# Optimization experiments

Measured on AMD Instinct MI355X. Metric: run time of the kernel, lower is better.

The kernel has to match this reference:

```python
import jax, jax.numpy as jnp
import numpy as np

H = 16  # hidden_size
D = 32  # input_size == output_size
B = 2048
T = 512


def _leaky(x):
    return jnp.where(x >= 0, x, 0.01 * x)  # nn.LeakyReLU default slope


def _lstm_cell(x, h, c, Wih, Whh, bih, bhh):
    # torch.nn.LSTMCell gate order: i, f, g, o
    g = x @ Wih.T + h @ Whh.T + bih + bhh  # [B, 4H]
    i, f, gg, o = jnp.split(g, 4, axis=-1)
    i = jax.nn.sigmoid(i)
    f = jax.nn.sigmoid(f)
    gg = jnp.tanh(gg)
    o = jax.nn.sigmoid(o)
    c = f * c + i * gg
    h = o * jnp.tanh(c)
    return h, c


def setup_inputs() -> dict:
    key = jax.random.key(0)
    ks = jax.random.split(key, 20)
    s = 1.0 / np.sqrt(H)
    u = lambda k, shape: jax.random.uniform(k, shape, jnp.float32, -s, s)
    return {
        "seq": jax.random.normal(ks[0], (B, T, D), jnp.float32),
        "pre_w1": u(ks[1], (H, D)), "pre_b1": u(ks[2], (H,)),
        "pre_w2": u(ks[3], (H, H)), "pre_b2": u(ks[4], (H,)),
        "pre_w3": u(ks[5], (H, H)), "pre_b3": u(ks[6], (H,)),
        "enc_Wih": u(ks[7], (4 * H, H)), "enc_Whh": u(ks[8], (4 * H, H)),
        "enc_bih": u(ks[9], (4 * H,)), "enc_bhh": u(ks[10], (4 * H,)),
        "h2l_w1": u(ks[11], (H, H)), "h2l_b1": u(ks[12], (H,)),
        "h2l_w2": u(ks[13], (H, H)), "h2l_b2": u(ks[14], (H,)),
        "post_w": u(ks[15], (D, H)), "post_b": u(ks[16], (D,)),
    }


def reference(seq, pre_w1, pre_b1, pre_w2, pre_b2, pre_w3, pre_b3,
              enc_Wih, enc_Whh, enc_bih, enc_bhh,
              h2l_w1, h2l_b1, h2l_w2, h2l_b2, post_w, post_b):
    Bx = seq.shape[0]
    # pre MLP: Linear -> LeakyReLU -> Linear -> LeakyReLU -> Linear
    x = _leaky(seq @ pre_w1.T + pre_b1)
    x = _leaky(x @ pre_w2.T + pre_b2)
    x = x @ pre_w3.T + pre_b3  # [B, T, H]

    start0 = x[:, -1, :]
    h0 = jnp.zeros((Bx, H), seq.dtype)
    c0 = jnp.zeros((Bx, H), seq.dtype)

    # encoder loop over time (serial)
    def enc_step(carry, xt):
        h, c = carry
        h, c = _lstm_cell(xt, h, c, enc_Wih, enc_Whh, enc_bih, enc_bhh)
        return (h, c), None

    (h, c), _ = jax.lax.scan(enc_step, (h0, c0), jnp.swapaxes(x, 0, 1))

    # decoder loop (note: source reuses self.encoder cell here)
    def dec_step(carry, _):
        h, c, start = carry
        h, c = _lstm_cell(start, h, c, enc_Wih, enc_Whh, enc_bih, enc_bhh)
        start = _leaky(h @ h2l_w1.T + h2l_b1) @ h2l_w2.T + h2l_b2
        out = h @ post_w.T + post_b  # [B, D]
        return (h, c, start), out

    _, outs = jax.lax.scan(dec_step, (h, c, start0), None, length=seq.shape[1])
    # outputs[:, -1 - i] = out_i  ->  reverse time, then [B, T, D]
    outputs = jnp.swapaxes(outs[::-1], 0, 1)
    return (outputs, outputs)
```

## Files before the change

### kernel.cpp

```cpp
#include <hip/hip_runtime.h>

#define T_LEN 512
#define OSTRIDE ((size_t)2048 * 512 * 32)

typedef float v2f __attribute__((ext_vector_type(2)));
#define PKFMA(a, b, c) __builtin_elementwise_fma((a), (b), (c))

__device__ __forceinline__ float rlf(float v, int l) {
  return __int_as_float(__builtin_amdgcn_readlane(__float_as_int(v), l));
}
#define QB(v, pat) __int_as_float(__builtin_amdgcn_mov_dpp(__float_as_int(v), (pat), 0xF, 0xF, false))

__global__ __launch_bounds__(64) void setup_kernel(
    const float* __restrict__ Wih, const float* __restrict__ bih,
    const float* __restrict__ bhh, const float* __restrict__ w3,
    const float* __restrict__ b3, float* __restrict__ Wz,
    float* __restrict__ Bz) {
  const int g = threadIdx.x;
  const float sK = ((g >> 4) == 2) ? 2.0f : -1.0f;
  float acc[16];
#pragma unroll
  for (int k = 0; k < 16; ++k) acc[k] = 0.f;
  float bz = bih[g] + bhh[g];
#pragma unroll
  for (int j = 0; j < 16; ++j) {
    const float wij = Wih[g * 16 + j];
#pragma unroll
    for (int k = 0; k < 16; ++k)
      acc[k] = __builtin_fmaf(wij, w3[j * 16 + k], acc[k]);
    bz = __builtin_fmaf(wij, b3[j], bz);
  }
#pragma unroll
  for (int k = 0; k < 16; ++k) Wz[g * 16 + k] = sK * acc[k];
  Bz[g] = sK * bz;
}

__global__ __launch_bounds__(256) void prenet_y2_kernel(
    const float* __restrict__ seq,
    const float* __restrict__ w1, const float* __restrict__ b1,
    const float* __restrict__ w2, const float* __restrict__ b2,
    const float* __restrict__ w3, const float* __restrict__ b3,
    float* __restrict__ y2g, float* __restrict__ xstart) {
  const int tid = threadIdx.x;
  const size_t r = (size_t)blockIdx.x * 256 + tid;

  const float* sp = seq + r * 32;
  float in[32];
#pragma unroll
  for (int q = 0; q < 8; ++q) {
    float4 v = ((const float4*)sp)[q];
    in[q * 4 + 0] = v.x;
    in[q * 4 + 1] = v.y;
    in[q * 4 + 2] = v.z;
    in[q * 4 + 3] = v.w;
  }

  float y1[16];
#pragma unroll
  for (int j = 0; j < 16; ++j) {
    float a0 = b1[j], a1 = 0.f, a2 = 0.f, a3 = 0.f;
#pragma unroll
    for (int k = 0; k < 32; k += 4) {
      a0 = __builtin_fmaf(w1[j * 32 + k + 0], in[k + 0], a0);
      a1 = __builtin_fmaf(w1[j * 32 + k + 1], in[k + 1], a1);
      a2 = __builtin_fmaf(w1[j * 32 + k + 2], in[k + 2], a2);
      a3 = __builtin_fmaf(w1[j * 32 + k + 3], in[k + 3], a3);
    }
    float s = (a0 + a1) + (a2 + a3);
    y1[j] = s >= 0.f ? s : 0.01f * s;
  }

  float y2[16];
#pragma unroll
  for (int j = 0; j < 16; ++j) {
    float a0 = b2[j], a1 = 0.f, a2 = 0.f, a3 = 0.f;
#pragma unroll
    for (int k = 0; k < 16; k += 4) {
      a0 = __builtin_fmaf(w2[j * 16 + k + 0], y1[k + 0], a0);
      a1 = __builtin_fmaf(w2[j * 16 + k + 1], y1[k + 1], a1);
      a2 = __builtin_fmaf(w2[j * 16 + k + 2], y1[k + 2], a2);
      a3 = __builtin_fmaf(w2[j * 16 + k + 3], y1[k + 3], a3);
    }
    float s = (a0 + a1) + (a2 + a3);
    y2[j] = s >= 0.f ? s : 0.01f * s;
  }

  float* op = y2g + r * 16;
#pragma unroll
  for (int q = 0; q < 4; ++q)
    ((float4*)op)[q] = make_float4(y2[q * 4 + 0], y2[q * 4 + 1],
                                   y2[q * 4 + 2], y2[q * 4 + 3]);

  if ((r & (T_LEN - 1)) == (T_LEN - 1)) {
    float y3[16];
#pragma unroll
    for (int j = 0; j < 16; ++j) {
      float a0 = b3[j], a1 = 0.f, a2 = 0.f, a3 = 0.f;
#pragma unroll
      for (int k = 0; k < 16; k += 4) {
        a0 = __builtin_fmaf(w3[j * 16 + k + 0], y2[k + 0], a0);
        a1 = __builtin_fmaf(w3[j * 16 + k + 1], y2[k + 1], a1);
        a2 = __builtin_fmaf(w3[j * 16 + k + 2], y2[k + 2], a2);
        a3 = __builtin_fmaf(w3[j * 16 + k + 3], y2[k + 3], a3);
      }
      y3[j] = (a0 + a1) + (a2 + a3);
    }
    float* xs = xstart + (r >> 9) * 16;
#pragma unroll
    for (int q = 0; q < 4; ++q)
      ((float4*)xs)[q] = make_float4(y3[q * 4 + 0], y3[q * 4 + 1],
                                     y3[q * 4 + 2], y3[q * 4 + 3]);
  }
}

#define ACTBODY()                                                           \
  do {                                                                      \
    float ee = __expf(g);                                                   \
    float rr = __builtin_amdgcn_rcpf(1.0f + ee);                            \
    float act = __builtin_fmaf(sa, rr, sb);                                 \
    float ii = QB(act, 0x00);                                               \
    float ff = QB(act, 0x55);                                               \
    float gg = QB(act, 0xAA);                                               \
    float oo = QB(act, 0xFF);                                               \
    c = __builtin_fmaf(ff, c, ii * gg);                                     \
    float th = __builtin_fmaf(                                              \
        -2.0f, __builtin_amdgcn_rcpf(1.0f + __expf(c + c)), 1.0f);          \
    h = oo * th;                                                            \
    _Pragma("unroll") for (int m = 0; m < 8; ++m) {                         \
      hk2[m].x = rlf(h, 8 * m);                                             \
      hk2[m].y = rlf(h, 8 * m + 4);                                         \
    }                                                                       \
  } while (0)

#define CELLZ(ZV)                                                           \
  do {                                                                      \
    v2f A, Bv;                                                              \
    A.x = (ZV); A.y = 0.f; Bv.x = 0.f; Bv.y = 0.f;                          \
    _Pragma("unroll") for (int m = 0; m < 8; m += 2) {                      \
      A = PKFMA(whh2[m], hk2[m], A);                                        \
      Bv = PKFMA(whh2[m + 1], hk2[m + 1], Bv);                              \
    }                                                                       \
    float g = (A.x + A.y) + (Bv.x + Bv.y);                                  \
    ACTBODY();                                                              \
  } while (0)

#define CELL(WX2, XA2, BB)                                                  \
  do {                                                                      \
    v2f A, Bv;                                                              \
    A.x = (BB); A.y = 0.f; Bv.x = 0.f; Bv.y = 0.f;                          \
    _Pragma("unroll") for (int m = 0; m < 8; m += 2) {                      \
      A = PKFMA(WX2[m], XA2[m], A);                                         \
      Bv = PKFMA(WX2[m + 1], XA2[m + 1], Bv);                               \
    }                                                                       \
    _Pragma("unroll") for (int m = 0; m < 8; m += 2) {                      \
      A = PKFMA(whh2[m], hk2[m], A);                                        \
      Bv = PKFMA(whh2[m + 1], hk2[m + 1], Bv);                              \
    }                                                                       \
    float g = (A.x + A.y) + (Bv.x + Bv.y);                                  \
    ACTBODY();                                                              \
  } while (0)

#define ZGEMV(YQ, OUTV)                                                     \
  do {                                                                      \
    v2f A, Bv;                                                              \
    A.x = bz; A.y = 0.f; Bv.x = 0.f; Bv.y = 0.f;                            \
    _Pragma("unroll") for (int q = 0; q < 4; ++q) {                         \
      float4 v = (YQ)[q];                                                   \
      v2f ylo, yhi;                                                         \
      ylo.x = v.x; ylo.y = v.y; yhi.x = v.z; yhi.y = v.w;                   \
      A = PKFMA(wz2[2 * q + 0], ylo, A);                                    \
      Bv = PKFMA(wz2[2 * q + 1], yhi, Bv);                                  \
    }                                                                       \
    OUTV = (A.x + A.y) + (Bv.x + Bv.y);                                     \
  } while (0)

__global__ __launch_bounds__(256, 2) void lstm_rec_z_kernel(
    const float* __restrict__ Whh, const float* __restrict__ Wih,
    const float* __restrict__ bih, const float* __restrict__ bhh,
    const float* __restrict__ hw1, const float* __restrict__ hb1,
    const float* __restrict__ hw2, const float* __restrict__ hb2,
    const float* __restrict__ pw, const float* __restrict__ pb,
    const float* __restrict__ Wz, const float* __restrict__ Bz,
    const float* __restrict__ y2g, const float* __restrict__ xstart,
    float* __restrict__ out) {
  const int lane = threadIdx.x & 63;
  const int bu =
      __builtin_amdgcn_readfirstlane(blockIdx.x * 4 + (threadIdx.x >> 6));
  const int hr = lane >> 2;
  const int gi = (lane & 3) * 16 + hr;
  const bool isT = (lane & 3) == 2;

  const float sK = isT ? 2.0f : -1.0f;
  const float sa = isT ? -2.0f : 1.0f;
  const float sb = isT ? 1.0f : 0.0f;

  v2f whh2[8];
#pragma unroll
  for (int m = 0; m < 8; ++m) {
    whh2[m].x = Whh[gi * 16 + 2 * m + 0] * sK;
    whh2[m].y = Whh[gi * 16 + 2 * m + 1] * sK;
  }

  v2f wz2[8];
  {
    const float4* wzv = (const float4*)(Wz + gi * 16);
#pragma unroll
    for (int q = 0; q < 4; ++q) {
      float4 v = wzv[q];
      wz2[2 * q + 0].x = v.x;
      wz2[2 * q + 0].y = v.y;
      wz2[2 * q + 1].x = v.z;
      wz2[2 * q + 1].y = v.w;
    }
  }
  const float bz = Bz[gi];

  float h = 0.f, c = 0.f;
  v2f hk2[8];
#pragma unroll
  for (int m = 0; m < 8; ++m) { hk2[m].x = 0.f; hk2[m].y = 0.f; }

  const float4* yb = (const float4*)(y2g + (size_t)bu * (T_LEN * 16));
  float4 yq[4][4];
#pragma unroll
  for (int u = 0; u < 4; ++u) {
#pragma unroll
    for (int q = 0; q < 4; ++q) yq[u][q] = yb[u * 4 + q];
  }
  __builtin_amdgcn_sched_barrier(0);

  float zcur;
  ZGEMV(yq[0], zcur);

  for (int t0 = 0; t0 < T_LEN; t0 += 4) {
#pragma unroll
    for (int u = 0; u < 4; ++u) {
      float znext;
      ZGEMV(yq[(u + 1) & 3], znext);
      CELLZ(zcur);
      int tn = t0 + u + 4;
      tn = tn < T_LEN ? tn : (T_LEN - 1);
#pragma unroll
      for (int q = 0; q < 4; ++q) yq[u][q] = yb[(size_t)tn * 4 + q];
      __builtin_amdgcn_sched_barrier(0);
      zcur = znext;
    }
  }

  v2f wih2[8];
#pragma unroll
  for (int m = 0; m < 8; ++m) {
    wih2[m].x = Wih[gi * 16 + 2 * m + 0] * sK;
    wih2[m].y = Wih[gi * 16 + 2 * m + 1] * sK;
  }
  const float bias = (bih[gi] + bhh[gi]) * sK;

  const int mrow = (lane < 32) ? lane : (lane & 15);
  const float* msrc = (lane < 32) ? (pw + mrow * 16) : (hw1 + mrow * 16);
  const float mbias = (lane < 32) ? pb[mrow] : hb1[mrow];
  const float sl = (lane < 32) ? 1.0f : 0.01f;
  v2f mr2[8];
#pragma unroll
  for (int m = 0; m < 8; ++m) {
    mr2[m].x = msrc[2 * m + 0];
    mr2[m].y = msrc[2 * m + 1];
  }

  float Mr[16];
#pragma unroll
  for (int k = 0; k < 16; ++k) Mr[k] = 0.f;
#pragma unroll
  for (int j = 0; j < 16; ++j) {
    const float wj = (j & 1) ? wih2[j >> 1].y : wih2[j >> 1].x;
#pragma unroll
    for (int k = 0; k < 16; ++k)
      Mr[k] = __builtin_fmaf(wj, hw2[j * 16 + k], Mr[k]);
  }
  float mbias2 = bias;
#pragma unroll
  for (int j = 0; j < 16; ++j) {
    const float wj = (j & 1) ? wih2[j >> 1].y : wih2[j >> 1].x;
    mbias2 = __builtin_fmaf(wj, hb2[j], mbias2);
  }
  v2f Mr2[8];
#pragma unroll
  for (int m = 0; m < 8; ++m) {
    Mr2[m].x = Mr[2 * m + 0];
    Mr2[m].y = Mr[2 * m + 1];
  }

  v2f xk2[8];
  {
    const float* src = xstart + (size_t)bu * 16;
#pragma unroll
    for (int m = 0; m < 8; ++m) {
      xk2[m].x = src[2 * m + 0];
      xk2[m].y = src[2 * m + 1];
    }
  }

  const size_t obase = (size_t)bu * (T_LEN * 32) + (lane & 31);

  CELL(wih2, xk2, bias);

  for (int t = 0; t < T_LEN; ++t) {
    v2f P, Q;
    P.x = mbias; P.y = 0.f; Q.x = 0.f; Q.y = 0.f;
#pragma unroll
    for (int m = 0; m < 8; m += 2) {
      P = PKFMA(mr2[m], hk2[m], P);
      Q = PKFMA(mr2[m + 1], hk2[m + 1], Q);
    }
    float y0 = (P.x + P.y) + (Q.x + Q.y);
    float yv = fmaxf(y0, y0 * sl);

    if (lane < 32) {
      const size_t off = obase + (size_t)(T_LEN - 1 - t) * 32;
      out[off] = yv;
      out[off + OSTRIDE] = yv;
    }

    if (t + 1 < T_LEN) {
      v2f uk2[8];
#pragma unroll
      for (int m = 0; m < 8; ++m) {
        uk2[m].x = rlf(yv, 32 + 2 * m + 0);
        uk2[m].y = rlf(yv, 32 + 2 * m + 1);
      }
      CELL(Mr2, uk2, mbias2);
    }
  }
}

__device__ __forceinline__ void prenet_row(
    const float* __restrict__ sp,
    const float* __restrict__ w1, const float* __restrict__ b1,
    const float* __restrict__ w2, const float* __restrict__ b2,
    const float* __restrict__ w3, const float* __restrict__ b3,
    float y3[16]) {
  float in[32];
#pragma unroll
  for (int q = 0; q < 8; ++q) {
    float4 v = ((const float4*)sp)[q];
    in[q * 4 + 0] = v.x;
    in[q * 4 + 1] = v.y;
    in[q * 4 + 2] = v.z;
    in[q * 4 + 3] = v.w;
  }
  float y1[16];
#pragma unroll
  for (int j = 0; j < 16; ++j) {
    float a0 = b1[j], a1 = 0.f, a2 = 0.f, a3 = 0.f;
#pragma unroll
    for (int k = 0; k < 32; k += 4) {
      a0 = __builtin_fmaf(w1[j * 32 + k + 0], in[k + 0], a0);
      a1 = __builtin_fmaf(w1[j * 32 + k + 1], in[k + 1], a1);
      a2 = __builtin_fmaf(w1[j * 32 + k + 2], in[k + 2], a2);
      a3 = __builtin_fmaf(w1[j * 32 + k + 3], in[k + 3], a3);
    }
    float s = (a0 + a1) + (a2 + a3);
    y1[j] = s >= 0.f ? s : 0.01f * s;
  }
  float y2[16];
#pragma unroll
  for (int j = 0; j < 16; ++j) {
    float a0 = b2[j], a1 = 0.f, a2 = 0.f, a3 = 0.f;
#pragma unroll
    for (int k = 0; k < 16; k += 4) {
      a0 = __builtin_fmaf(w2[j * 16 + k + 0], y1[k + 0], a0);
      a1 = __builtin_fmaf(w2[j * 16 + k + 1], y1[k + 1], a1);
      a2 = __builtin_fmaf(w2[j * 16 + k + 2], y1[k + 2], a2);
      a3 = __builtin_fmaf(w2[j * 16 + k + 3], y1[k + 3], a3);
    }
    float s = (a0 + a1) + (a2 + a3);
    y2[j] = s >= 0.f ? s : 0.01f * s;
  }
#pragma unroll
  for (int j = 0; j < 16; ++j) {
    float a0 = b3[j], a1 = 0.f, a2 = 0.f, a3 = 0.f;
#pragma unroll
    for (int k = 0; k < 16; k += 4) {
      a0 = __builtin_fmaf(w3[j * 16 + k + 0], y2[k + 0], a0);
      a1 = __builtin_fmaf(w3[j * 16 + k + 1], y2[k + 1], a1);
      a2 = __builtin_fmaf(w3[j * 16 + k + 2], y2[k + 2], a2);
      a3 = __builtin_fmaf(w3[j * 16 + k + 3], y2[k + 3], a3);
    }
    y3[j] = (a0 + a1) + (a2 + a3);
  }
}

__global__ __launch_bounds__(256) void prenet_kernel(
    const float* __restrict__ seq,
    const float* __restrict__ w1, const float* __restrict__ b1,
    const float* __restrict__ w2, const float* __restrict__ b2,
    const float* __restrict__ w3, const float* __restrict__ b3,
    float* __restrict__ xws) {
  const size_t r = (size_t)blockIdx.x * 256 + threadIdx.x;
  float y3[16];
  prenet_row(seq + r * 32, w1, b1, w2, b2, w3, b3, y3);
  float* op = xws + r * 16;
#pragma unroll
  for (int q = 0; q < 4; ++q)
    ((float4*)op)[q] =
        make_float4(y3[q * 4 + 0], y3[q * 4 + 1], y3[q * 4 + 2], y3[q * 4 + 3]);
}

__global__ __launch_bounds__(256, 2) void lstm_rec_kernel(
    const float* __restrict__ Wih, const float* __restrict__ Whh,
    const float* __restrict__ bih, const float* __restrict__ bhh,
    const float* __restrict__ hw1, const float* __restrict__ hb1,
    const float* __restrict__ hw2, const float* __restrict__ hb2,
    const float* __restrict__ pw, const float* __restrict__ pb,
    const float* __restrict__ xws, float* __restrict__ out) {
  const int lane = threadIdx.x & 63;
  const int bu =
      __builtin_amdgcn_readfirstlane(blockIdx.x * 4 + (threadIdx.x >> 6));
  const int hr = lane >> 2;
  const int gi = (lane & 3) * 16 + hr;
  const bool isT = (lane & 3) == 2;

  const float sK = isT ? 2.0f : -1.0f;
  const float sa = isT ? -2.0f : 1.0f;
  const float sb = isT ? 1.0f : 0.0f;

  v2f wih2[8], whh2[8];
#pragma unroll
  for (int m = 0; m < 8; ++m) {
    wih2[m].x = Wih[gi * 16 + 2 * m + 0] * sK;
    wih2[m].y = Wih[gi * 16 + 2 * m + 1] * sK;
    whh2[m].x = Whh[gi * 16 + 2 * m + 0] * sK;
    whh2[m].y = Whh[gi * 16 + 2 * m + 1] * sK;
  }
  const float bias = (bih[gi] + bhh[gi]) * sK;

  float h = 0.f, c = 0.f;
  v2f hk2[8];
#pragma unroll
  for (int m = 0; m < 8; ++m) { hk2[m].x = 0.f; hk2[m].y = 0.f; }

  const float* xb = xws + (size_t)bu * (T_LEN * 16);

  v2f xA2[8], xB2[8];
#pragma unroll
  for (int m = 0; m < 8; ++m) {
    xA2[m].x = xb[2 * m + 0];
    xA2[m].y = xb[2 * m + 1];
  }
  for (int t = 0; t < T_LEN; t += 2) {
    const float* n1 = xb + (size_t)(t + 1) * 16;
#pragma unroll
    for (int m = 0; m < 8; ++m) {
      xB2[m].x = n1[2 * m + 0];
      xB2[m].y = n1[2 * m + 1];
    }
    CELL(wih2, xA2, bias);
    const int t2 = (t + 2 < T_LEN) ? (t + 2) : (T_LEN - 1);
    const float* n2 = xb + (size_t)t2 * 16;
#pragma unroll
    for (int m = 0; m < 8; ++m) {
      xA2[m].x = n2[2 * m + 0];
      xA2[m].y = n2[2 * m + 1];
    }
    CELL(wih2, xB2, bias);
  }

  const int mrow = (lane < 32) ? lane : (lane & 15);
  const float* msrc = (lane < 32) ? (pw + mrow * 16) : (hw1 + mrow * 16);
  const float mbias = (lane < 32) ? pb[mrow] : hb1[mrow];
  const float sl = (lane < 32) ? 1.0f : 0.01f;
  v2f mr2[8];
#pragma unroll
  for (int m = 0; m < 8; ++m) {
    mr2[m].x = msrc[2 * m + 0];
    mr2[m].y = msrc[2 * m + 1];
  }

  float Mr[16];
#pragma unroll
  for (int k = 0; k < 16; ++k) Mr[k] = 0.f;
#pragma unroll
  for (int j = 0; j < 16; ++j) {
    const float wj = (j & 1) ? wih2[j >> 1].y : wih2[j >> 1].x;
#pragma unroll
    for (int k = 0; k < 16; ++k)
      Mr[k] = __builtin_fmaf(wj, hw2[j * 16 + k], Mr[k]);
  }
  float mbias2 = bias;
#pragma unroll
  for (int j = 0; j < 16; ++j) {
    const float wj = (j & 1) ? wih2[j >> 1].y : wih2[j >> 1].x;
    mbias2 = __builtin_fmaf(wj, hb2[j], mbias2);
  }
  v2f Mr2[8];
#pragma unroll
  for (int m = 0; m < 8; ++m) {
    Mr2[m].x = Mr[2 * m + 0];
    Mr2[m].y = Mr[2 * m + 1];
  }

  v2f xk2[8];
  {
    const float* src = xb + (size_t)(T_LEN - 1) * 16;
#pragma unroll
    for (int m = 0; m < 8; ++m) {
      xk2[m].x = src[2 * m + 0];
      xk2[m].y = src[2 * m + 1];
    }
  }

  const size_t obase = (size_t)bu * (T_LEN * 32) + (lane & 31);

  CELL(wih2, xk2, bias);

  for (int t = 0; t < T_LEN; ++t) {
    v2f P, Q;
    P.x = mbias; P.y = 0.f; Q.x = 0.f; Q.y = 0.f;
#pragma unroll
    for (int m = 0; m < 8; m += 2) {
      P = PKFMA(mr2[m], hk2[m], P);
      Q = PKFMA(mr2[m + 1], hk2[m + 1], Q);
    }
    float y0 = (P.x + P.y) + (Q.x + Q.y);
    float yv = fmaxf(y0, y0 * sl);

    if (lane < 32) {
      const size_t off = obase + (size_t)(T_LEN - 1 - t) * 32;
      out[off] = yv;
      out[off + OSTRIDE] = yv;
    }

    if (t + 1 < T_LEN) {
      v2f uk2[8];
#pragma unroll
      for (int m = 0; m < 8; ++m) {
        uk2[m].x = rlf(yv, 32 + 2 * m + 0);
        uk2[m].y = rlf(yv, 32 + 2 * m + 1);
      }
      CELL(Mr2, uk2, mbias2);
    }
  }
}

extern "C" void kernel_launch(void* const* d_in, const int* in_sizes, int n_in,
                              void* d_out, int out_size, void* d_ws, size_t ws_size,
                              hipStream_t stream) {
  const float* seq = (const float*)d_in[0];
  const float* pre_w1 = (const float*)d_in[1];
  const float* pre_b1 = (const float*)d_in[2];
  const float* pre_w2 = (const float*)d_in[3];
  const float* pre_b2 = (const float*)d_in[4];
  const float* pre_w3 = (const float*)d_in[5];
  const float* pre_b3 = (const float*)d_in[6];
  const float* enc_Wih = (const float*)d_in[7];
  const float* enc_Whh = (const float*)d_in[8];
  const float* enc_bih = (const float*)d_in[9];
  const float* enc_bhh = (const float*)d_in[10];
  const float* h2l_w1 = (const float*)d_in[11];
  const float* h2l_b1 = (const float*)d_in[12];
  const float* h2l_w2 = (const float*)d_in[13];
  const float* h2l_b2 = (const float*)d_in[14];
  const float* post_w = (const float*)d_in[15];
  const float* post_b = (const float*)d_in[16];

  const size_t y2bytes = (size_t)2048 * 512 * 16 * 4;
  const size_t xsbytes = (size_t)2048 * 16 * 4;
  const size_t wzbytes = 64 * 16 * 4;
  const size_t need = y2bytes + xsbytes + wzbytes + 64 * 4;

  if (ws_size >= need) {
    float* y2g = (float*)d_ws;
    float* xstart = (float*)((char*)d_ws + y2bytes);
    float* Wz = (float*)((char*)d_ws + y2bytes + xsbytes);
    float* Bz = (float*)((char*)d_ws + y2bytes + xsbytes + wzbytes);

    setup_kernel<<<dim3(1), dim3(64), 0, stream>>>(
        enc_Wih, enc_bih, enc_bhh, pre_w3, pre_b3, Wz, Bz);

    prenet_y2_kernel<<<dim3(4096), dim3(256), 0, stream>>>(
        seq, pre_w1, pre_b1, pre_w2, pre_b2, pre_w3, pre_b3, y2g, xstart);

    lstm_rec_z_kernel<<<dim3(512), dim3(256), 0, stream>>>(
        enc_Whh, enc_Wih, enc_bih, enc_bhh, h2l_w1, h2l_b1, h2l_w2, h2l_b2,
        post_w, post_b, Wz, Bz, y2g, xstart, (float*)d_out);
  } else {
    float* xws = (float*)d_ws;

    prenet_kernel<<<dim3(4096), dim3(256), 0, stream>>>(
        seq, pre_w1, pre_b1, pre_w2, pre_b2, pre_w3, pre_b3, xws);

    lstm_rec_kernel<<<dim3(512), dim3(256), 0, stream>>>(
        enc_Wih, enc_Whh, enc_bih, enc_bhh, h2l_w1, h2l_b1, h2l_w2, h2l_b2,
        post_w, post_b, xws, (float*)d_out);
  }
}
```

Before: 712.9 us.

## Fuse prenet MLP into recurrent LSTM kernel with per-wave LDS chunks

Replaces the separate setup and prenet kernels, and the global y2 workspace, with a single kernel. Each wave computes the first two prenet layers for its own batch row in chunks of 128 timesteps, stages them in LDS, and then runs the encoder recurrence from LDS. The folded Wih·W3 weights and the decoder start vector are now computed inside the kernel. This removes the large global round trip for y2 and two kernel launches. In exchange, the prenet work now runs inside each latency-bound recurrence wave instead of a wide parallel kernel, and the kernel uses more LDS and registers.

```diff
diff --git a/kernel.cpp b/kernel.cpp
--- a/kernel.cpp
+++ b/kernel.cpp
@@ -11,107 +11,6 @@
 }
 #define QB(v, pat) __int_as_float(__builtin_amdgcn_mov_dpp(__float_as_int(v), (pat), 0xF, 0xF, false))
 
-__global__ __launch_bounds__(64) void setup_kernel(
-    const float* __restrict__ Wih, const float* __restrict__ bih,
-    const float* __restrict__ bhh, const float* __restrict__ w3,
-    const float* __restrict__ b3, float* __restrict__ Wz,
-    float* __restrict__ Bz) {
-  const int g = threadIdx.x;
-  const float sK = ((g >> 4) == 2) ? 2.0f : -1.0f;
-  float acc[16];
-#pragma unroll
-  for (int k = 0; k < 16; ++k) acc[k] = 0.f;
-  float bz = bih[g] + bhh[g];
-#pragma unroll
-  for (int j = 0; j < 16; ++j) {
-    const float wij = Wih[g * 16 + j];
-#pragma unroll
-    for (int k = 0; k < 16; ++k)
-      acc[k] = __builtin_fmaf(wij, w3[j * 16 + k], acc[k]);
-    bz = __builtin_fmaf(wij, b3[j], bz);
-  }
-#pragma unroll
-  for (int k = 0; k < 16; ++k) Wz[g * 16 + k] = sK * acc[k];
-  Bz[g] = sK * bz;
-}
-
-__global__ __launch_bounds__(256) void prenet_y2_kernel(
-    const float* __restrict__ seq,
-    const float* __restrict__ w1, const float* __restrict__ b1,
-    const float* __restrict__ w2, const float* __restrict__ b2,
-    const float* __restrict__ w3, const float* __restrict__ b3,
-    float* __restrict__ y2g, float* __restrict__ xstart) {
-  const int tid = threadIdx.x;
-  const size_t r = (size_t)blockIdx.x * 256 + tid;
-
-  const float* sp = seq + r * 32;
-  float in[32];
-#pragma unroll
-  for (int q = 0; q < 8; ++q) {
-    float4 v = ((const float4*)sp)[q];
-    in[q * 4 + 0] = v.x;
-    in[q * 4 + 1] = v.y;
-    in[q * 4 + 2] = v.z;
-    in[q * 4 + 3] = v.w;
-  }
-
-  float y1[16];
-#pragma unroll
-  for (int j = 0; j < 16; ++j) {
-    float a0 = b1[j], a1 = 0.f, a2 = 0.f, a3 = 0.f;
-#pragma unroll
-    for (int k = 0; k < 32; k += 4) {
-      a0 = __builtin_fmaf(w1[j * 32 + k + 0], in[k + 0], a0);
-      a1 = __builtin_fmaf(w1[j * 32 + k + 1], in[k + 1], a1);
-      a2 = __builtin_fmaf(w1[j * 32 + k + 2], in[k + 2], a2);
-      a3 = __builtin_fmaf(w1[j * 32 + k + 3], in[k + 3], a3);
-    }
-    float s = (a0 + a1) + (a2 + a3);
-    y1[j] = s >= 0.f ? s : 0.01f * s;
-  }
-
-  float y2[16];
-#pragma unroll
-  for (int j = 0; j < 16; ++j) {
-    float a0 = b2[j], a1 = 0.f, a2 = 0.f, a3 = 0.f;
-#pragma unroll
-    for (int k = 0; k < 16; k += 4) {
-      a0 = __builtin_fmaf(w2[j * 16 + k + 0], y1[k + 0], a0);
-      a1 = __builtin_fmaf(w2[j * 16 + k + 1], y1[k + 1], a1);
-      a2 = __builtin_fmaf(w2[j * 16 + k + 2], y1[k + 2], a2);
-      a3 = __builtin_fmaf(w2[j * 16 + k + 3], y1[k + 3], a3);
-    }
-    float s = (a0 + a1) + (a2 + a3);
-    y2[j] = s >= 0.f ? s : 0.01f * s;
-  }
-
-  float* op = y2g + r * 16;
-#pragma unroll
-  for (int q = 0; q < 4; ++q)
-    ((float4*)op)[q] = make_float4(y2[q * 4 + 0], y2[q * 4 + 1],
-                                   y2[q * 4 + 2], y2[q * 4 + 3]);
-
-  if ((r & (T_LEN - 1)) == (T_LEN - 1)) {
-    float y3[16];
-#pragma unroll
-    for (int j = 0; j < 16; ++j) {
-      float a0 = b3[j], a1 = 0.f, a2 = 0.f, a3 = 0.f;
-#pragma unroll
-      for (int k = 0; k < 16; k += 4) {
-        a0 = __builtin_fmaf(w3[j * 16 + k + 0], y2[k + 0], a0);
-        a1 = __builtin_fmaf(w3[j * 16 + k + 1], y2[k + 1], a1);
-        a2 = __builtin_fmaf(w3[j * 16 + k + 2], y2[k + 2], a2);
-        a3 = __builtin_fmaf(w3[j * 16 + k + 3], y2[k + 3], a3);
-      }
-      y3[j] = (a0 + a1) + (a2 + a3);
-    }
-    float* xs = xstart + (r >> 9) * 16;
-#pragma unroll
-    for (int q = 0; q < 4; ++q)
-      ((float4*)xs)[q] = make_float4(y3[q * 4 + 0], y3[q * 4 + 1],
-                                     y3[q * 4 + 2], y3[q * 4 + 3]);
-  }
-}
 
 #define ACTBODY()                                                           \
   do {                                                                      \
@@ -174,18 +73,66 @@
     OUTV = (A.x + A.y) + (Bv.x + Bv.y);                                     \
   } while (0)
 
-__global__ __launch_bounds__(256, 2) void lstm_rec_z_kernel(
-    const float* __restrict__ Whh, const float* __restrict__ Wih,
+#define PHASEA_ROW(SR, ROWOFF)                                              \
+  do {                                                                      \
+    float in[32];                                                           \
+    _Pragma("unroll") for (int q = 0; q < 8; ++q) {                         \
+      in[q * 4 + 0] = SR[q].x;                                              \
+      in[q * 4 + 1] = SR[q].y;                                              \
+      in[q * 4 + 2] = SR[q].z;                                              \
+      in[q * 4 + 3] = SR[q].w;                                              \
+    }                                                                       \
+    float y1[16];                                                           \
+    _Pragma("unroll") for (int j = 0; j < 16; ++j) {                        \
+      float a0 = b1[j], a1 = 0.f, a2 = 0.f, a3 = 0.f;                       \
+      _Pragma("unroll") for (int k = 0; k < 32; k += 4) {                   \
+        a0 = __builtin_fmaf(w1[j * 32 + k + 0], in[k + 0], a0);             \
+        a1 = __builtin_fmaf(w1[j * 32 + k + 1], in[k + 1], a1);             \
+        a2 = __builtin_fmaf(w1[j * 32 + k + 2], in[k + 2], a2);             \
+        a3 = __builtin_fmaf(w1[j * 32 + k + 3], in[k + 3], a3);             \
+      }                                                                     \
+      float s = (a0 + a1) + (a2 + a3);                                      \
+      y1[j] = s >= 0.f ? s : 0.01f * s;                                     \
+    }                                                                       \
+    float y2[16];                                                           \
+    _Pragma("unroll") for (int j = 0; j < 16; ++j) {                        \
+      float a0 = b2[j], a1 = 0.f, a2 = 0.f, a3 = 0.f;                       \
+      _Pragma("unroll") for (int k = 0; k < 16; k += 4) {                   \
+        a0 = __builtin_fmaf(w2[j * 16 + k + 0], y1[k + 0], a0);             \
+        a1 = __builtin_fmaf(w2[j * 16 + k + 1], y1[k + 1], a1);             \
+        a2 = __builtin_fmaf(w2[j * 16 + k + 2], y1[k + 2], a2);             \
+        a3 = __builtin_fmaf(w2[j * 16 + k + 3], y1[k + 3], a3);             \
+      }                                                                     \
+      float s = (a0 + a1) + (a2 + a3);                                      \
+      y2[j] = s >= 0.f ? s : 0.01f * s;                                     \
+    }                                                                       \
+    float* yp = myy + (ROWOFF) * 20;                                        \
+    _Pragma("unroll") for (int q = 0; q < 4; ++q)                           \
+      ((float4*)yp)[q] = make_float4(y2[q * 4 + 0], y2[q * 4 + 1],          \
+                                     y2[q * 4 + 2], y2[q * 4 + 3]);         \
+  } while (0)
+
+#define LOADSEQ(DST, ROW)                                                   \
+  do {                                                                      \
+    const float4* sp4 = (const float4*)(sb0 + (size_t)(ROW) * 32);          \
+    _Pragma("unroll") for (int q = 0; q < 8; ++q) DST[q] = sp4[q];          \
+  } while (0)
+
+__global__ __launch_bounds__(256, 2) void lstm_fused_kernel(
+    const float* __restrict__ seq,
+    const float* __restrict__ w1, const float* __restrict__ b1,
+    const float* __restrict__ w2, const float* __restrict__ b2,
+    const float* __restrict__ w3, const float* __restrict__ b3,
+    const float* __restrict__ Wih, const float* __restrict__ Whh,
     const float* __restrict__ bih, const float* __restrict__ bhh,
     const float* __restrict__ hw1, const float* __restrict__ hb1,
     const float* __restrict__ hw2, const float* __restrict__ hb2,
     const float* __restrict__ pw, const float* __restrict__ pb,
-    const float* __restrict__ Wz, const float* __restrict__ Bz,
-    const float* __restrict__ y2g, const float* __restrict__ xstart,
     float* __restrict__ out) {
+  __shared__ float y2s[4][128 * 20];
   const int lane = threadIdx.x & 63;
-  const int bu =
-      __builtin_amdgcn_readfirstlane(blockIdx.x * 4 + (threadIdx.x >> 6));
+  const int wid = threadIdx.x >> 6;
+  const int bu = __builtin_amdgcn_readfirstlane(blockIdx.x * 4 + wid);
   const int hr = lane >> 2;
   const int gi = (lane & 3) * 16 + hr;
   const bool isT = (lane & 3) == 2;
@@ -202,48 +149,76 @@
   }
 
   v2f wz2[8];
+  float bz;
   {
-    const float4* wzv = (const float4*)(Wz + gi * 16);
-#pragma unroll
-    for (int q = 0; q < 4; ++q) {
-      float4 v = wzv[q];
-      wz2[2 * q + 0].x = v.x;
-      wz2[2 * q + 0].y = v.y;
-      wz2[2 * q + 1].x = v.z;
-      wz2[2 * q + 1].y = v.w;
-    }
-  }
-  const float bz = Bz[gi];
+    float acc[16];
+#pragma unroll
+    for (int k = 0; k < 16; ++k) acc[k] = 0.f;
+    float bz0 = bih[gi] + bhh[gi];
+#pragma unroll
+    for (int j = 0; j < 16; ++j) {
+      const float wij = Wih[gi * 16 + j];
+#pragma unroll
+      for (int k = 0; k < 16; ++k)
+        acc[k] = __builtin_fmaf(wij, w3[j * 16 + k], acc[k]);
+      bz0 = __builtin_fmaf(wij, b3[j], bz0);
+    }
+#pragma unroll
+    for (int m = 0; m < 8; ++m) {
+      wz2[m].x = sK * acc[2 * m + 0];
+      wz2[m].y = sK * acc[2 * m + 1];
+    }
+    bz = sK * bz0;
+  }
 
   float h = 0.f, c = 0.f;
   v2f hk2[8];
 #pragma unroll
   for (int m = 0; m < 8; ++m) { hk2[m].x = 0.f; hk2[m].y = 0.f; }
 
-  const float4* yb = (const float4*)(y2g + (size_t)bu * (T_LEN * 16));
-  float4 yq[4][4];
-#pragma unroll
-  for (int u = 0; u < 4; ++u) {
-#pragma unroll
-    for (int q = 0; q < 4; ++q) yq[u][q] = yb[u * 4 + q];
-  }
+  const float* sb0 = seq + ((size_t)bu * T_LEN) * 32;
+  float* myy = &y2s[wid][0];
+
+  float4 sA[8], sB[8];
+  LOADSEQ(sA, lane);
+  LOADSEQ(sB, lane + 64);
   __builtin_amdgcn_sched_barrier(0);
 
-  float zcur;
-  ZGEMV(yq[0], zcur);
-
-  for (int t0 = 0; t0 < T_LEN; t0 += 4) {
+  for (int ch = 0; ch < 4; ++ch) {
+    PHASEA_ROW(sA, lane);
+    PHASEA_ROW(sB, lane + 64);
+    if (ch < 3) {
+      const int rbase = (ch + 1) * 128 + lane;
+      LOADSEQ(sA, rbase);
+      LOADSEQ(sB, rbase + 64);
+    }
+    __builtin_amdgcn_sched_barrier(0);
+
+    float4 yq[4][4];
 #pragma unroll
     for (int u = 0; u < 4; ++u) {
-      float znext;
-      ZGEMV(yq[(u + 1) & 3], znext);
-      CELLZ(zcur);
-      int tn = t0 + u + 4;
-      tn = tn < T_LEN ? tn : (T_LEN - 1);
-#pragma unroll
-      for (int q = 0; q < 4; ++q) yq[u][q] = yb[(size_t)tn * 4 + q];
-      __builtin_amdgcn_sched_barrier(0);
-      zcur = znext;
+#pragma unroll
+      for (int q = 0; q < 4; ++q) yq[u][q] = ((float4*)(myy + u * 20))[q];
+    }
+    __builtin_amdgcn_sched_barrier(0);
+
+    float zcur;
+    ZGEMV(yq[0], zcur);
+
+    for (int t0 = 0; t0 < 128; t0 += 4) {
+#pragma unroll
+      for (int u = 0; u < 4; ++u) {
+        float znext;
+        ZGEMV(yq[(u + 1) & 3], znext);
+        CELLZ(zcur);
+        int tn = t0 + u + 4;
+        tn = tn < 128 ? tn : 127;
+#pragma unroll
+        for (int q = 0; q < 4; ++q)
+          yq[u][q] = ((float4*)(myy + tn * 20))[q];
+        __builtin_amdgcn_sched_barrier(0);
+        zcur = znext;
+      }
     }
   }
 
@@ -291,220 +266,32 @@
 
   v2f xk2[8];
   {
-    const float* src = xstart + (size_t)bu * 16;
+    float yl[16];
+#pragma unroll
+    for (int q = 0; q < 4; ++q) {
+      float4 v = ((float4*)(myy + 127 * 20))[q];
+      yl[q * 4 + 0] = v.x;
+      yl[q * 4 + 1] = v.y;
+      yl[q * 4 + 2] = v.z;
+      yl[q * 4 + 3] = v.w;
+    }
+    float y3[16];
+#pragma unroll
+    for (int j = 0; j < 16; ++j) {
+      float a0 = b3[j], a1 = 0.f, a2 = 0.f, a3 = 0.f;
+#pragma unroll
+      for (int k = 0; k < 16; k += 4) {
+        a0 = __builtin_fmaf(w3[j * 16 + k + 0], yl[k + 0], a0);
+        a1 = __builtin_fmaf(w3[j * 16 + k + 1], yl[k + 1], a1);
+        a2 = __builtin_fmaf(w3[j * 16 + k + 2], yl[k + 2], a2);
+        a3 = __builtin_fmaf(w3[j * 16 + k + 3], yl[k + 3], a3);
+      }
+      y3[j] = (a0 + a1) + (a2 + a3);
+    }
 #pragma unroll
     for (int m = 0; m < 8; ++m) {
-      xk2[m].x = src[2 * m + 0];
-      xk2[m].y = src[2 * m + 1];
-    }
-  }
-
-  const size_t obase = (size_t)bu * (T_LEN * 32) + (lane & 31);
-
-  CELL(wih2, xk2, bias);
-
-  for (int t = 0; t < T_LEN; ++t) {
-    v2f P, Q;
-    P.x = mbias; P.y = 0.f; Q.x = 0.f; Q.y = 0.f;
-#pragma unroll
-    for (int m = 0; m < 8; m += 2) {
-      P = PKFMA(mr2[m], hk2[m], P);
-      Q = PKFMA(mr2[m + 1], hk2[m + 1], Q);
-    }
-    float y0 = (P.x + P.y) + (Q.x + Q.y);
-    float yv = fmaxf(y0, y0 * sl);
-
-    if (lane < 32) {
-      const size_t off = obase + (size_t)(T_LEN - 1 - t) * 32;
-      out[off] = yv;
-      out[off + OSTRIDE] = yv;
-    }
-
-    if (t + 1 < T_LEN) {
-      v2f uk2[8];
-#pragma unroll
-      for (int m = 0; m < 8; ++m) {
-        uk2[m].x = rlf(yv, 32 + 2 * m + 0);
-        uk2[m].y = rlf(yv, 32 + 2 * m + 1);
-      }
-      CELL(Mr2, uk2, mbias2);
-    }
-  }
-}
-
-__device__ __forceinline__ void prenet_row(
-    const float* __restrict__ sp,
-    const float* __restrict__ w1, const float* __restrict__ b1,
-    const float* __restrict__ w2, const float* __restrict__ b2,
-    const float* __restrict__ w3, const float* __restrict__ b3,
-    float y3[16]) {
-  float in[32];
-#pragma unroll
-  for (int q = 0; q < 8; ++q) {
-    float4 v = ((const float4*)sp)[q];
-    in[q * 4 + 0] = v.x;
-    in[q * 4 + 1] = v.y;
-    in[q * 4 + 2] = v.z;
-    in[q * 4 + 3] = v.w;
-  }
-  float y1[16];
-#pragma unroll
-  for (int j = 0; j < 16; ++j) {
-    float a0 = b1[j], a1 = 0.f, a2 = 0.f, a3 = 0.f;
-#pragma unroll
-    for (int k = 0; k < 32; k += 4) {
-      a0 = __builtin_fmaf(w1[j * 32 + k + 0], in[k + 0], a0);
-      a1 = __builtin_fmaf(w1[j * 32 + k + 1], in[k + 1], a1);
-      a2 = __builtin_fmaf(w1[j * 32 + k + 2], in[k + 2], a2);
-      a3 = __builtin_fmaf(w1[j * 32 + k + 3], in[k + 3], a3);
-    }
-    float s = (a0 + a1) + (a2 + a3);
-    y1[j] = s >= 0.f ? s : 0.01f * s;
-  }
-  float y2[16];
-#pragma unroll
-  for (int j = 0; j < 16; ++j) {
-    float a0 = b2[j], a1 = 0.f, a2 = 0.f, a3 = 0.f;
-#pragma unroll
-    for (int k = 0; k < 16; k += 4) {
-      a0 = __builtin_fmaf(w2[j * 16 + k + 0], y1[k + 0], a0);
-      a1 = __builtin_fmaf(w2[j * 16 + k + 1], y1[k + 1], a1);
-      a2 = __builtin_fmaf(w2[j * 16 + k + 2], y1[k + 2], a2);
-      a3 = __builtin_fmaf(w2[j * 16 + k + 3], y1[k + 3], a3);
-    }
-    float s = (a0 + a1) + (a2 + a3);
-    y2[j] = s >= 0.f ? s : 0.01f * s;
-  }
-#pragma unroll
-  for (int j = 0; j < 16; ++j) {
-    float a0 = b3[j], a1 = 0.f, a2 = 0.f, a3 = 0.f;
-#pragma unroll
-    for (int k = 0; k < 16; k += 4) {
-      a0 = __builtin_fmaf(w3[j * 16 + k + 0], y2[k + 0], a0);
-      a1 = __builtin_fmaf(w3[j * 16 + k + 1], y2[k + 1], a1);
-      a2 = __builtin_fmaf(w3[j * 16 + k + 2], y2[k + 2], a2);
-      a3 = __builtin_fmaf(w3[j * 16 + k + 3], y2[k + 3], a3);
-    }
-    y3[j] = (a0 + a1) + (a2 + a3);
-  }
-}
-
-__global__ __launch_bounds__(256) void prenet_kernel(
-    const float* __restrict__ seq,
-    const float* __restrict__ w1, const float* __restrict__ b1,
-    const float* __restrict__ w2, const float* __restrict__ b2,
-    const float* __restrict__ w3, const float* __restrict__ b3,
-    float* __restrict__ xws) {
-  const size_t r = (size_t)blockIdx.x * 256 + threadIdx.x;
-  float y3[16];
-  prenet_row(seq + r * 32, w1, b1, w2, b2, w3, b3, y3);
-  float* op = xws + r * 16;
-#pragma unroll
-  for (int q = 0; q < 4; ++q)
-    ((float4*)op)[q] =
-        make_float4(y3[q * 4 + 0], y3[q * 4 + 1], y3[q * 4 + 2], y3[q * 4 + 3]);
-}
-
-__global__ __launch_bounds__(256, 2) void lstm_rec_kernel(
-    const float* __restrict__ Wih, const float* __restrict__ Whh,
-    const float* __restrict__ bih, const float* __restrict__ bhh,
-    const float* __restrict__ hw1, const float* __restrict__ hb1,
-    const float* __restrict__ hw2, const float* __restrict__ hb2,
-    const float* __restrict__ pw, const float* __restrict__ pb,
-    const float* __restrict__ xws, float* __restrict__ out) {
-  const int lane = threadIdx.x & 63;
-  const int bu =
-      __builtin_amdgcn_readfirstlane(blockIdx.x * 4 + (threadIdx.x >> 6));
-  const int hr = lane >> 2;
-  const int gi = (lane & 3) * 16 + hr;
-  const bool isT = (lane & 3) == 2;
-
-  const float sK = isT ? 2.0f : -1.0f;
-  const float sa = isT ? -2.0f : 1.0f;
-  const float sb = isT ? 1.0f : 0.0f;
-
-  v2f wih2[8], whh2[8];
-#pragma unroll
-  for (int m = 0; m < 8; ++m) {
-    wih2[m].x = Wih[gi * 16 + 2 * m + 0] * sK;
-    wih2[m].y = Wih[gi * 16 + 2 * m + 1] * sK;
-    whh2[m].x = Whh[gi * 16 + 2 * m + 0] * sK;
-    whh2[m].y = Whh[gi * 16 + 2 * m + 1] * sK;
-  }
-  const float bias = (bih[gi] + bhh[gi]) * sK;
-
-  float h = 0.f, c = 0.f;
-  v2f hk2[8];
-#pragma unroll
-  for (int m = 0; m < 8; ++m) { hk2[m].x = 0.f; hk2[m].y = 0.f; }
-
-  const float* xb = xws + (size_t)bu * (T_LEN * 16);
-
-  v2f xA2[8], xB2[8];
-#pragma unroll
-  for (int m = 0; m < 8; ++m) {
-    xA2[m].x = xb[2 * m + 0];
-    xA2[m].y = xb[2 * m + 1];
-  }
-  for (int t = 0; t < T_LEN; t += 2) {
-    const float* n1 = xb + (size_t)(t + 1) * 16;
-#pragma unroll
-    for (int m = 0; m < 8; ++m) {
-      xB2[m].x = n1[2 * m + 0];
-      xB2[m].y = n1[2 * m + 1];
-    }
-    CELL(wih2, xA2, bias);
-    const int t2 = (t + 2 < T_LEN) ? (t + 2) : (T_LEN - 1);
-    const float* n2 = xb + (size_t)t2 * 16;
-#pragma unroll
-    for (int m = 0; m < 8; ++m) {
-      xA2[m].x = n2[2 * m + 0];
-      xA2[m].y = n2[2 * m + 1];
-    }
-    CELL(wih2, xB2, bias);
-  }
-
-  const int mrow = (lane < 32) ? lane : (lane & 15);
-  const float* msrc = (lane < 32) ? (pw + mrow * 16) : (hw1 + mrow * 16);
-  const float mbias = (lane < 32) ? pb[mrow] : hb1[mrow];
-  const float sl = (lane < 32) ? 1.0f : 0.01f;
-  v2f mr2[8];
-#pragma unroll
-  for (int m = 0; m < 8; ++m) {
-    mr2[m].x = msrc[2 * m + 0];
-    mr2[m].y = msrc[2 * m + 1];
-  }
-
-  float Mr[16];
-#pragma unroll
-  for (int k = 0; k < 16; ++k) Mr[k] = 0.f;
-#pragma unroll
-  for (int j = 0; j < 16; ++j) {
-    const float wj = (j & 1) ? wih2[j >> 1].y : wih2[j >> 1].x;
-#pragma unroll
-    for (int k = 0; k < 16; ++k)
-      Mr[k] = __builtin_fmaf(wj, hw2[j * 16 + k], Mr[k]);
-  }
-  float mbias2 = bias;
-#pragma unroll
-  for (int j = 0; j < 16; ++j) {
-    const float wj = (j & 1) ? wih2[j >> 1].y : wih2[j >> 1].x;
-    mbias2 = __builtin_fmaf(wj, hb2[j], mbias2);
-  }
-  v2f Mr2[8];
-#pragma unroll
-  for (int m = 0; m < 8; ++m) {
-    Mr2[m].x = Mr[2 * m + 0];
-    Mr2[m].y = Mr[2 * m + 1];
-  }
-
-  v2f xk2[8];
-  {
-    const float* src = xb + (size_t)(T_LEN - 1) * 16;
-#pragma unroll
-    for (int m = 0; m < 8; ++m) {
-      xk2[m].x = src[2 * m + 0];
-      xk2[m].y = src[2 * m + 1];
+      xk2[m].x = y3[2 * m + 0];
+      xk2[m].y = y3[2 * m + 1];
     }
   }
 
@@ -562,34 +349,11 @@
   const float* post_w = (const float*)d_in[15];
   const float* post_b = (const float*)d_in[16];
 
-  const size_t y2bytes = (size_t)2048 * 512 * 16 * 4;
-  const size_t xsbytes = (size_t)2048 * 16 * 4;
-  const size_t wzbytes = 64 * 16 * 4;
-  const size_t need = y2bytes + xsbytes + wzbytes + 64 * 4;
-
-  if (ws_size >= need) {
-    float* y2g = (float*)d_ws;
-    float* xstart = (float*)((char*)d_ws + y2bytes);
-    float* Wz = (float*)((char*)d_ws + y2bytes + xsbytes);
-    float* Bz = (float*)((char*)d_ws + y2bytes + xsbytes + wzbytes);
-
-    setup_kernel<<<dim3(1), dim3(64), 0, stream>>>(
-        enc_Wih, enc_bih, enc_bhh, pre_w3, pre_b3, Wz, Bz);
-
-    prenet_y2_kernel<<<dim3(4096), dim3(256), 0, stream>>>(
-        seq, pre_w1, pre_b1, pre_w2, pre_b2, pre_w3, pre_b3, y2g, xstart);
-
-    lstm_rec_z_kernel<<<dim3(512), dim3(256), 0, stream>>>(
-        enc_Whh, enc_Wih, enc_bih, enc_bhh, h2l_w1, h2l_b1, h2l_w2, h2l_b2,
-        post_w, post_b, Wz, Bz, y2g, xstart, (float*)d_out);
-  } else {
-    float* xws = (float*)d_ws;
-
-    prenet_kernel<<<dim3(4096), dim3(256), 0, stream>>>(
-        seq, pre_w1, pre_b1, pre_w2, pre_b2, pre_w3, pre_b3, xws);
-
-    lstm_rec_kernel<<<dim3(512), dim3(256), 0, stream>>>(
-        enc_Wih, enc_Whh, enc_bih, enc_bhh, h2l_w1, h2l_b1, h2l_w2, h2l_b2,
-        post_w, post_b, xws, (float*)d_out);
-  }
+  (void)d_ws;
+  (void)ws_size;
+
+  lstm_fused_kernel<<<dim3(512), dim3(256), 0, stream>>>(
+      seq, pre_w1, pre_b1, pre_w2, pre_b2, pre_w3, pre_b3, enc_Wih, enc_Whh,
+      enc_bih, enc_bhh, h2l_w1, h2l_b1, h2l_w2, h2l_b2, post_w, post_b,
+      (float*)d_out);
 }
```

Result: slower. 775.0 us (+8.7%).
